# Performance work log

Hardware: AMD Instinct MI355X
Metric: run time of the kernel (lower is better)

Reference implementation:

```python
import jax, jax.numpy as jnp
import numpy as np

BLOCK = 128  # block_size=(128,128) from MoeFP8Matmul
E, H, I = 8, 2048, 2816  # experts, hidden, intermediate
T, K = 512, 2  # tokens, top-k

_FP8 = getattr(jnp, "float8_e4m3fn", jnp.float32)

def _dequant(w, s):
    # w: [N, Kd] fp8 values (stored fp32), s: [N//128, Kd//128] inverse scales
    s_full = jnp.repeat(jnp.repeat(s, BLOCK, axis=-2), BLOCK, axis=-1)
    return w * s_full

def setup_inputs() -> dict:
    key = jax.random.key(0)
    ks = jax.random.split(key, 7)
    x = jax.random.normal(ks[0], (T, H), dtype=jnp.float32)
    topk_ids = jax.random.randint(ks[1], (T, K), 0, E, dtype=jnp.int64)
    topk_weights = jax.random.uniform(ks[2], (T, K), dtype=jnp.float32)
    # fp8-representable weight values (round-trip through e4m3)
    w13 = (jax.random.normal(ks[3], (E, 2 * I, H), dtype=jnp.float32) * 0.5)
    w13_fp8 = w13.astype(_FP8).astype(jnp.float32)
    w2 = (jax.random.normal(ks[4], (E, H, I), dtype=jnp.float32) * 0.5)
    w2_fp8 = w2.astype(_FP8).astype(jnp.float32)
    w13_scale = jax.random.uniform(ks[5], (E, (2 * I) // BLOCK, H // BLOCK),
                                   dtype=jnp.float32, minval=0.5, maxval=1.5)
    w2_scale = jax.random.uniform(ks[6], (E, H // BLOCK, I // BLOCK),
                                  dtype=jnp.float32, minval=0.5, maxval=1.5)
    return {"x": x, "topk_ids": topk_ids, "topk_weights": topk_weights,
            "w13_fp8": w13_fp8, "w13_scale": w13_scale,
            "w2_fp8": w2_fp8, "w2_scale": w2_scale}

def reference(x, topk_ids, topk_weights, w13_fp8, w13_scale, w2_fp8, w2_scale):
    # Per-expert block-FP8 dequant then grouped SwiGLU MoE GEMM, weighted-summed by router.
    out = jnp.zeros_like(x)
    for e in range(E):  # small fixed expert count
        W13 = _dequant(w13_fp8[e], w13_scale[e])   # [2I, H]
        W2 = _dequant(w2_fp8[e], w2_scale[e])      # [H, I]
        h = x @ W13.T                              # [T, 2I]
        gate, up = jnp.split(h, 2, axis=-1)
        act = jax.nn.silu(gate) * up               # [T, I]
        oe = act @ W2.T                            # [T, H]
        coef = jnp.sum(jnp.where(topk_ids == e, topk_weights, 0.0), axis=-1)  # [T]
        out = out + coef[:, None] * oe
    return out
```

## Files before the change

### kernel.cpp

```cpp
#include <hip/hip_runtime.h>
#include <hip/hip_bf16.h>
#include <cstdint>
#include <cstddef>

#define E_   8
#define H_   2048
#define I_   2816
#define T_   512
#define NPAIR 1024

#define TM   192
#define TN   32
#define BK   64
#define LDSB 72
#define MT_  3

typedef __attribute__((ext_vector_type(8))) short          bf16x8;
typedef __attribute__((ext_vector_type(4))) float          f32x4;
typedef __attribute__((ext_vector_type(8))) unsigned short u16x8;

__device__ __forceinline__ unsigned short f2bf(float f){
  union { float f; unsigned u; } a; a.f = f;
  unsigned u = a.u;
  unsigned r = u + 0x7fffu + ((u >> 16) & 1u);
  return (unsigned short)(r >> 16);
}

__global__ void route_kernel(const int* __restrict__ ids,
                             int* __restrict__ offs, int* __restrict__ ptok,
                             int* __restrict__ sop){
  __shared__ int scnt[E_];
  __shared__ int scur[E_];
  const int tid = threadIdx.x;
  if (tid < E_) scnt[tid] = 0;
  __syncthreads();
  const int e = ids[tid];
  atomicAdd(&scnt[e], 1);
  __syncthreads();
  if (tid == 0){
    int s = 0;
    for (int i = 0; i < E_; i++){ offs[i] = s; scur[i] = s; s += scnt[i]; }
    offs[E_] = s;
  }
  __syncthreads();
  const int pos = atomicAdd(&scur[e], 1);
  ptok[pos] = tid >> 1;
  sop[tid]  = pos;
}

__global__ void prep_kernel(const float* __restrict__ x, const int* __restrict__ ptok,
                            unsigned short* __restrict__ xg){
  const int slot = blockIdx.x;
  const int tok  = ptok[slot];
  const int k0   = threadIdx.x * 8;
  const float4 v0 = *(const float4*)(x + (size_t)tok*H_ + k0);
  const float4 v1 = *(const float4*)(x + (size_t)tok*H_ + k0 + 4);
  u16x8 o;
  o[0]=f2bf(v0.x); o[1]=f2bf(v0.y); o[2]=f2bf(v0.z); o[3]=f2bf(v0.w);
  o[4]=f2bf(v1.x); o[5]=f2bf(v1.y); o[6]=f2bf(v1.z); o[7]=f2bf(v1.w);
  *(u16x8*)(xg + (size_t)slot*H_ + k0) = o;
}

__global__ __launch_bounds__(256, 3)
void gemm1_kernel(const unsigned short* __restrict__ xg, const float* __restrict__ w13,
                  const float* __restrict__ s13, const int* __restrict__ offs,
                  unsigned short* __restrict__ act)
{
  const int e   = blockIdx.z;
  const int off = offs[e];
  const int cnt = offs[e+1] - off;
  const int m0  = blockIdx.y * TM;
  if (m0 >= cnt) return;
  const int rows = min(TM, cnt - m0);
  const int nb   = blockIdx.x * TN;

  __shared__ __align__(16) unsigned short Bs[2][2*TN][LDSB];

  const int tid  = threadIdx.x;
  const int wave = tid >> 6;
  const int lane = tid & 63;
  const int quad = lane >> 4;
  const int l16  = lane & 15;

  const float* w13e = w13 + (size_t)e * (2*I_) * H_;
  const float* s13e = s13 + (size_t)e * (2*I_/128) * (H_/128);

  const int br = tid >> 2;
  const int bc = tid & 3;
  const int grow = (br < TN) ? (nb + br) : (I_ + nb + (br - TN));
  const float* bp = w13e + (size_t)grow * H_;
  const int srow  = ((br < TN) ? 0 : (I_/128)) + (nb >> 7);

  const unsigned short* aP[MT_];
  #pragma unroll
  for (int mt = 0; mt < MT_; mt++){
    int sl = off + m0 + wave*(TM/4) + mt*16 + l16;
    sl = min(sl, NPAIR - 1);
    aP[mt] = xg + (size_t)sl * H_;
  }

  f32x4 acc[2][MT_][2];
  #pragma unroll
  for (int h = 0; h < 2; h++)
    #pragma unroll
    for (int mt = 0; mt < MT_; mt++)
      #pragma unroll
      for (int nt = 0; nt < 2; nt++)
        acc[h][mt][nt] = (f32x4){0.f, 0.f, 0.f, 0.f};

  float4 pb[4];
  #pragma unroll
  for (int j = 0; j < 4; j++) pb[j] = *(const float4*)(bp + (bc*4 + j)*4);
  {
    const float s = s13e[srow*(H_/128)];
    u16x8 wv0, wv1;
    wv0[0]=f2bf(pb[0].x*s); wv0[1]=f2bf(pb[0].y*s); wv0[2]=f2bf(pb[0].z*s); wv0[3]=f2bf(pb[0].w*s);
    wv0[4]=f2bf(pb[1].x*s); wv0[5]=f2bf(pb[1].y*s); wv0[6]=f2bf(pb[1].z*s); wv0[7]=f2bf(pb[1].w*s);
    wv1[0]=f2bf(pb[2].x*s); wv1[1]=f2bf(pb[2].y*s); wv1[2]=f2bf(pb[2].z*s); wv1[3]=f2bf(pb[2].w*s);
    wv1[4]=f2bf(pb[3].x*s); wv1[5]=f2bf(pb[3].y*s); wv1[6]=f2bf(pb[3].z*s); wv1[7]=f2bf(pb[3].w*s);
    *(u16x8*)&Bs[0][br][bc*16]     = wv0;
    *(u16x8*)&Bs[0][br][bc*16 + 8] = wv1;
  }
  __syncthreads();

  int cur = 0;
  for (int kb = 0; kb < H_; kb += BK){
    const bool more = (kb + BK) < H_;
    if (more){
      #pragma unroll
      for (int j = 0; j < 4; j++) pb[j] = *(const float4*)(bp + kb + BK + (bc*4 + j)*4);
    }
    bf16x8 af[2][MT_];
    #pragma unroll
    for (int kk = 0; kk < 2; kk++)
      #pragma unroll
      for (int mt = 0; mt < MT_; mt++)
        af[kk][mt] = *(const bf16x8*)(aP[mt] + kb + kk*32 + quad*8);

    #pragma unroll
    for (int kk = 0; kk < 2; kk++){
      #pragma unroll
      for (int hh = 0; hh < 2; hh++){
        #pragma unroll
        for (int nt = 0; nt < 2; nt++){
          bf16x8 bv = *(const bf16x8*)&Bs[cur][hh*TN + nt*16 + l16][kk*32 + quad*8];
          #pragma unroll
          for (int mt = 0; mt < MT_; mt++)
            acc[hh][mt][nt] = __builtin_amdgcn_mfma_f32_16x16x32_bf16(af[kk][mt], bv, acc[hh][mt][nt], 0, 0, 0);
        }
      }
    }
    if (more){
      const float s = s13e[srow*(H_/128) + ((kb + BK) >> 7)];
      u16x8 wv0, wv1;
      wv0[0]=f2bf(pb[0].x*s); wv0[1]=f2bf(pb[0].y*s); wv0[2]=f2bf(pb[0].z*s); wv0[3]=f2bf(pb[0].w*s);
      wv0[4]=f2bf(pb[1].x*s); wv0[5]=f2bf(pb[1].y*s); wv0[6]=f2bf(pb[1].z*s); wv0[7]=f2bf(pb[1].w*s);
      wv1[0]=f2bf(pb[2].x*s); wv1[1]=f2bf(pb[2].y*s); wv1[2]=f2bf(pb[2].z*s); wv1[3]=f2bf(pb[2].w*s);
      wv1[4]=f2bf(pb[3].x*s); wv1[5]=f2bf(pb[3].y*s); wv1[6]=f2bf(pb[3].z*s); wv1[7]=f2bf(pb[3].w*s);
      *(u16x8*)&Bs[cur^1][br][bc*16]     = wv0;
      *(u16x8*)&Bs[cur^1][br][bc*16 + 8] = wv1;
      __syncthreads();
      cur ^= 1;
    }
  }

  #pragma unroll
  for (int mt = 0; mt < MT_; mt++){
    #pragma unroll
    for (int nt = 0; nt < 2; nt++){
      #pragma unroll
      for (int r = 0; r < 4; r++){
        const int m = wave*(TM/4) + mt*16 + quad*4 + r;
        if (m < rows){
          const float g = acc[0][mt][nt][r];
          const float u = acc[1][mt][nt][r];
          const float sg = g / (1.f + __expf(-g));
          act[(size_t)(off + m0 + m)*I_ + (nb + nt*16 + l16)] = f2bf(sg * u);
        }
      }
    }
  }
}

__global__ __launch_bounds__(256, 4)
void gemm2_kernel(const unsigned short* __restrict__ act, const float* __restrict__ w2,
                  const float* __restrict__ s2, const int* __restrict__ offs,
                  float* __restrict__ buf)
{
  const int e   = blockIdx.z;
  const int off = offs[e];
  const int cnt = offs[e+1] - off;
  const int m0  = blockIdx.y * TM;
  if (m0 >= cnt) return;
  const int rows = min(TM, cnt - m0);
  const int nb   = blockIdx.x * TN;

  __shared__ __align__(16) unsigned short Bs[2][TN][LDSB];

  const int tid  = threadIdx.x;
  const int wave = tid >> 6;
  const int lane = tid & 63;
  const int quad = lane >> 4;
  const int l16  = lane & 15;

  const float* w2e = w2 + (size_t)e * H_ * I_;
  const float* s2e = s2 + (size_t)e * (H_/128) * (I_/128);

  const int br = tid >> 3;
  const int bc = tid & 7;
  const float* bp = w2e + (size_t)(nb + br) * I_;
  const int srow  = nb >> 7;

  const unsigned short* aP[MT_];
  #pragma unroll
  for (int mt = 0; mt < MT_; mt++){
    int sl = off + m0 + wave*(TM/4) + mt*16 + l16;
    sl = min(sl, NPAIR - 1);
    aP[mt] = act + (size_t)sl * I_;
  }

  f32x4 acc[MT_][2];
  #pragma unroll
  for (int mt = 0; mt < MT_; mt++)
    #pragma unroll
    for (int nt = 0; nt < 2; nt++)
      acc[mt][nt] = (f32x4){0.f, 0.f, 0.f, 0.f};

  float4 pb[2];
  #pragma unroll
  for (int j = 0; j < 2; j++) pb[j] = *(const float4*)(bp + (bc*2 + j)*4);
  {
    const float s = s2e[srow*(I_/128)];
    u16x8 wv;
    wv[0]=f2bf(pb[0].x*s); wv[1]=f2bf(pb[0].y*s); wv[2]=f2bf(pb[0].z*s); wv[3]=f2bf(pb[0].w*s);
    wv[4]=f2bf(pb[1].x*s); wv[5]=f2bf(pb[1].y*s); wv[6]=f2bf(pb[1].z*s); wv[7]=f2bf(pb[1].w*s);
    *(u16x8*)&Bs[0][br][bc*8] = wv;
  }
  __syncthreads();

  int cur = 0;
  for (int kb = 0; kb < I_; kb += BK){
    const bool more = (kb + BK) < I_;
    if (more){
      #pragma unroll
      for (int j = 0; j < 2; j++) pb[j] = *(const float4*)(bp + kb + BK + (bc*2 + j)*4);
    }
    bf16x8 af[2][MT_];
    #pragma unroll
    for (int kk = 0; kk < 2; kk++)
      #pragma unroll
      for (int mt = 0; mt < MT_; mt++)
        af[kk][mt] = *(const bf16x8*)(aP[mt] + kb + kk*32 + quad*8);

    #pragma unroll
    for (int kk = 0; kk < 2; kk++){
      #pragma unroll
      for (int nt = 0; nt < 2; nt++){
        bf16x8 bv = *(const bf16x8*)&Bs[cur][nt*16 + l16][kk*32 + quad*8];
        #pragma unroll
        for (int mt = 0; mt < MT_; mt++)
          acc[mt][nt] = __builtin_amdgcn_mfma_f32_16x16x32_bf16(af[kk][mt], bv, acc[mt][nt], 0, 0, 0);
      }
    }
    if (more){
      const float s = s2e[srow*(I_/128) + ((kb + BK) >> 7)];
      u16x8 wv;
      wv[0]=f2bf(pb[0].x*s); wv[1]=f2bf(pb[0].y*s); wv[2]=f2bf(pb[0].z*s); wv[3]=f2bf(pb[0].w*s);
      wv[4]=f2bf(pb[1].x*s); wv[5]=f2bf(pb[1].y*s); wv[6]=f2bf(pb[1].z*s); wv[7]=f2bf(pb[1].w*s);
      *(u16x8*)&Bs[cur^1][br][bc*8] = wv;
      __syncthreads();
      cur ^= 1;
    }
  }

  #pragma unroll
  for (int mt = 0; mt < MT_; mt++){
    #pragma unroll
    for (int nt = 0; nt < 2; nt++){
      #pragma unroll
      for (int r = 0; r < 4; r++){
        const int m = wave*(TM/4) + mt*16 + quad*4 + r;
        if (m < rows)
          buf[(size_t)(off + m0 + m)*H_ + (nb + nt*16 + l16)] = acc[mt][nt][r];
      }
    }
  }
}

__global__ void combine_kernel(const float* __restrict__ buf, const int* __restrict__ sop,
                               const float* __restrict__ tw, float* __restrict__ out){
  const int gid = blockIdx.x*256 + threadIdx.x;
  const int t = gid >> 9;
  const int c = gid & 511;
  const int s0 = sop[2*t], s1 = sop[2*t+1];
  const float w0 = tw[2*t], w1 = tw[2*t+1];
  const float4 v0 = ((const float4*)buf)[(size_t)s0*(H_/4) + c];
  const float4 v1 = ((const float4*)buf)[(size_t)s1*(H_/4) + c];
  float4 o;
  o.x = w0*v0.x + w1*v1.x;
  o.y = w0*v0.y + w1*v1.y;
  o.z = w0*v0.z + w1*v1.z;
  o.w = w0*v0.w + w1*v1.w;
  ((float4*)out)[gid] = o;
}

extern "C" void kernel_launch(void* const* d_in, const int* in_sizes, int n_in,
                              void* d_out, int out_size, void* d_ws, size_t ws_size,
                              hipStream_t stream){
  const float* x   = (const float*)d_in[0];
  const int*   ids = (const int*)  d_in[1];
  const float* tw  = (const float*)d_in[2];
  const float* w13 = (const float*)d_in[3];
  const float* s13 = (const float*)d_in[4];
  const float* w2  = (const float*)d_in[5];
  const float* s2  = (const float*)d_in[6];
  float* out = (float*)d_out;

  char* ws = (char*)d_ws;
  int* offs = (int*)ws;
  int* ptok = (int*)(ws + 64);
  int* sop  = (int*)(ws + 64 + 4096);
  unsigned short* xg  = (unsigned short*)(ws + 16384);
  float*          buf = (float*)(ws + 16384);
  unsigned short* act = (unsigned short*)(ws + 16384 + (size_t)NPAIR*H_*4);

  route_kernel  <<<1, NPAIR, 0, stream>>>(ids, offs, ptok, sop);
  prep_kernel   <<<NPAIR, 256, 0, stream>>>(x, ptok, xg);
  gemm1_kernel  <<<dim3(I_/TN, (NPAIR + TM - 1)/TM, E_), 256, 0, stream>>>(xg, w13, s13, offs, act);
  gemm2_kernel  <<<dim3(H_/TN, (NPAIR + TM - 1)/TM, E_), 256, 0, stream>>>(act, w2, s2, offs, buf);
  combine_kernel<<<(T_*H_/4)/256, 256, 0, stream>>>(buf, sop, tw, out);
}
```

Measured before the change: 793.0 us.

## Software-pipeline both MoE GEMMs with register double-buffering and LDS-only barriers

Restructures the K loops of both grouped GEMMs into a 2-way unrolled pipeline. Weight tiles are prefetched two steps ahead and activation fragments one step ahead in registers, and __syncthreads is replaced by a barrier that waits only on LDS counters, so global loads can stay in flight across the barrier. The bf16 conversion now uses packed HIP intrinsics, pointer offsets are hoisted out of the loop, and gemm2's launch bound drops to 3 blocks per SM to make room for the extra registers. The risk is higher register pressure and lower occupancy.

```diff
diff --git a/kernel.cpp b/kernel.cpp
--- a/kernel.cpp
+++ b/kernel.cpp
@@ -24,6 +24,20 @@
   unsigned u = a.u;
   unsigned r = u + 0x7fffu + ((u >> 16) & 1u);
   return (unsigned short)(r >> 16);
+}
+
+__device__ __forceinline__ void cvt4(u16x8& dst, int base, const float4 v, float s){
+  __hip_bfloat162 p0 = __float22bfloat162_rn(float2{v.x*s, v.y*s});
+  __hip_bfloat162 p1 = __float22bfloat162_rn(float2{v.z*s, v.w*s});
+  union { __hip_bfloat162 b; unsigned u; } a0{p0}, a1{p1};
+  dst[base+0] = (unsigned short)(a0.u & 0xffff);
+  dst[base+1] = (unsigned short)(a0.u >> 16);
+  dst[base+2] = (unsigned short)(a1.u & 0xffff);
+  dst[base+3] = (unsigned short)(a1.u >> 16);
+}
+
+__device__ __forceinline__ void sync_lds(){
+  asm volatile("s_waitcnt lgkmcnt(0)\n\ts_barrier" ::: "memory");
 }
 
 __global__ void route_kernel(const int* __restrict__ ids,
@@ -56,8 +70,8 @@
   const float4 v0 = *(const float4*)(x + (size_t)tok*H_ + k0);
   const float4 v1 = *(const float4*)(x + (size_t)tok*H_ + k0 + 4);
   u16x8 o;
-  o[0]=f2bf(v0.x); o[1]=f2bf(v0.y); o[2]=f2bf(v0.z); o[3]=f2bf(v0.w);
-  o[4]=f2bf(v1.x); o[5]=f2bf(v1.y); o[6]=f2bf(v1.z); o[7]=f2bf(v1.w);
+  cvt4(o, 0, v0, 1.f);
+  cvt4(o, 4, v1, 1.f);
   *(u16x8*)(xg + (size_t)slot*H_ + k0) = o;
 }
 
@@ -88,15 +102,15 @@
   const int br = tid >> 2;
   const int bc = tid & 3;
   const int grow = (br < TN) ? (nb + br) : (I_ + nb + (br - TN));
-  const float* bp = w13e + (size_t)grow * H_;
-  const int srow  = ((br < TN) ? 0 : (I_/128)) + (nb >> 7);
+  const float* bp = w13e + (size_t)grow * H_ + bc*16;
+  const int srow  = (((br < TN) ? 0 : (I_/128)) + (nb >> 7)) * (H_/128);
 
   const unsigned short* aP[MT_];
   #pragma unroll
   for (int mt = 0; mt < MT_; mt++){
     int sl = off + m0 + wave*(TM/4) + mt*16 + l16;
     sl = min(sl, NPAIR - 1);
-    aP[mt] = xg + (size_t)sl * H_;
+    aP[mt] = xg + (size_t)sl * H_ + quad*8;
   }
 
   f32x4 acc[2][MT_][2];
@@ -108,60 +122,60 @@
       for (int nt = 0; nt < 2; nt++)
         acc[h][mt][nt] = (f32x4){0.f, 0.f, 0.f, 0.f};
 
-  float4 pb[4];
-  #pragma unroll
-  for (int j = 0; j < 4; j++) pb[j] = *(const float4*)(bp + (bc*4 + j)*4);
-  {
-    const float s = s13e[srow*(H_/128)];
-    u16x8 wv0, wv1;
-    wv0[0]=f2bf(pb[0].x*s); wv0[1]=f2bf(pb[0].y*s); wv0[2]=f2bf(pb[0].z*s); wv0[3]=f2bf(pb[0].w*s);
-    wv0[4]=f2bf(pb[1].x*s); wv0[5]=f2bf(pb[1].y*s); wv0[6]=f2bf(pb[1].z*s); wv0[7]=f2bf(pb[1].w*s);
-    wv1[0]=f2bf(pb[2].x*s); wv1[1]=f2bf(pb[2].y*s); wv1[2]=f2bf(pb[2].z*s); wv1[3]=f2bf(pb[2].w*s);
-    wv1[4]=f2bf(pb[3].x*s); wv1[5]=f2bf(pb[3].y*s); wv1[6]=f2bf(pb[3].z*s); wv1[7]=f2bf(pb[3].w*s);
-    *(u16x8*)&Bs[0][br][bc*16]     = wv0;
-    *(u16x8*)&Bs[0][br][bc*16 + 8] = wv1;
-  }
-  __syncthreads();
-
-  int cur = 0;
-  for (int kb = 0; kb < H_; kb += BK){
-    const bool more = (kb + BK) < H_;
-    if (more){
-      #pragma unroll
-      for (int j = 0; j < 4; j++) pb[j] = *(const float4*)(bp + kb + BK + (bc*4 + j)*4);
-    }
-    bf16x8 af[2][MT_];
+  float4 R0[4], R1[4];
+  bf16x8 A0[2][MT_], A1[2][MT_];
+  float  sE, sO;
+
+  auto loadB = [&](int t, float4* R){
+    const float* p = bp + t*BK;
+    #pragma unroll
+    for (int j = 0; j < 4; j++) R[j] = *(const float4*)(p + j*4);
+  };
+  auto loadA = [&](int t, bf16x8 (*A)[MT_]){
     #pragma unroll
     for (int kk = 0; kk < 2; kk++)
       #pragma unroll
       for (int mt = 0; mt < MT_; mt++)
-        af[kk][mt] = *(const bf16x8*)(aP[mt] + kb + kk*32 + quad*8);
-
-    #pragma unroll
-    for (int kk = 0; kk < 2; kk++){
-      #pragma unroll
-      for (int hh = 0; hh < 2; hh++){
+        A[kk][mt] = *(const bf16x8*)(aP[mt] + t*BK + kk*32);
+  };
+  auto storeB = [&](const float4* R, float s, int buf){
+    u16x8 w0, w1;
+    cvt4(w0, 0, R[0], s); cvt4(w0, 4, R[1], s);
+    cvt4(w1, 0, R[2], s); cvt4(w1, 4, R[3], s);
+    *(u16x8*)&Bs[buf][br][bc*16]     = w0;
+    *(u16x8*)&Bs[buf][br][bc*16 + 8] = w1;
+  };
+  auto mfma = [&](int buf, bf16x8 (*A)[MT_]){
+    #pragma unroll
+    for (int kk = 0; kk < 2; kk++)
+      #pragma unroll
+      for (int hh = 0; hh < 2; hh++)
         #pragma unroll
         for (int nt = 0; nt < 2; nt++){
-          bf16x8 bv = *(const bf16x8*)&Bs[cur][hh*TN + nt*16 + l16][kk*32 + quad*8];
+          bf16x8 bv = *(const bf16x8*)&Bs[buf][hh*TN + nt*16 + l16][kk*32 + quad*8];
           #pragma unroll
           for (int mt = 0; mt < MT_; mt++)
-            acc[hh][mt][nt] = __builtin_amdgcn_mfma_f32_16x16x32_bf16(af[kk][mt], bv, acc[hh][mt][nt], 0, 0, 0);
+            acc[hh][mt][nt] = __builtin_amdgcn_mfma_f32_16x16x32_bf16(A[kk][mt], bv, acc[hh][mt][nt], 0, 0, 0);
         }
-      }
-    }
-    if (more){
-      const float s = s13e[srow*(H_/128) + ((kb + BK) >> 7)];
-      u16x8 wv0, wv1;
-      wv0[0]=f2bf(pb[0].x*s); wv0[1]=f2bf(pb[0].y*s); wv0[2]=f2bf(pb[0].z*s); wv0[3]=f2bf(pb[0].w*s);
-      wv0[4]=f2bf(pb[1].x*s); wv0[5]=f2bf(pb[1].y*s); wv0[6]=f2bf(pb[1].z*s); wv0[7]=f2bf(pb[1].w*s);
-      wv1[0]=f2bf(pb[2].x*s); wv1[1]=f2bf(pb[2].y*s); wv1[2]=f2bf(pb[2].z*s); wv1[3]=f2bf(pb[2].w*s);
-      wv1[4]=f2bf(pb[3].x*s); wv1[5]=f2bf(pb[3].y*s); wv1[6]=f2bf(pb[3].z*s); wv1[7]=f2bf(pb[3].w*s);
-      *(u16x8*)&Bs[cur^1][br][bc*16]     = wv0;
-      *(u16x8*)&Bs[cur^1][br][bc*16 + 8] = wv1;
-      __syncthreads();
-      cur ^= 1;
-    }
+  };
+
+  const int NITER = H_/BK;
+  loadB(0, R0); sE = s13e[srow];
+  loadB(1, R1); sO = s13e[srow];
+  loadA(0, A0);
+  storeB(R0, sE, 0);
+  sync_lds();
+
+  for (int i = 0; i < NITER; i += 2){
+    if (i+2 < NITER){ loadB(i+2, R0); sE = s13e[srow + ((i+2) >> 1)]; }
+    loadA(i+1, A1);
+    mfma(0, A0);
+    storeB(R1, sO, 1);
+    sync_lds();
+    if (i+3 < NITER){ loadB(i+3, R1); sO = s13e[srow + ((i+3) >> 1)]; }
+    if (i+2 < NITER) loadA(i+2, A0);
+    mfma(1, A1);
+    if (i+2 < NITER){ storeB(R0, sE, 0); sync_lds(); }
   }
 
   #pragma unroll
@@ -182,7 +196,7 @@
   }
 }
 
-__global__ __launch_bounds__(256, 4)
+__global__ __launch_bounds__(256, 3)
 void gemm2_kernel(const unsigned short* __restrict__ act, const float* __restrict__ w2,
                   const float* __restrict__ s2, const int* __restrict__ offs,
                   float* __restrict__ buf)
@@ -208,15 +222,15 @@
 
   const int br = tid >> 3;
   const int bc = tid & 7;
-  const float* bp = w2e + (size_t)(nb + br) * I_;
-  const int srow  = nb >> 7;
+  const float* bp = w2e + (size_t)(nb + br) * I_ + bc*8;
+  const int srow  = (nb >> 7) * (I_/128);
 
   const unsigned short* aP[MT_];
   #pragma unroll
   for (int mt = 0; mt < MT_; mt++){
     int sl = off + m0 + wave*(TM/4) + mt*16 + l16;
     sl = min(sl, NPAIR - 1);
-    aP[mt] = act + (size_t)sl * I_;
+    aP[mt] = act + (size_t)sl * I_ + quad*8;
   }
 
   f32x4 acc[MT_][2];
@@ -226,51 +240,56 @@
     for (int nt = 0; nt < 2; nt++)
       acc[mt][nt] = (f32x4){0.f, 0.f, 0.f, 0.f};
 
-  float4 pb[2];
-  #pragma unroll
-  for (int j = 0; j < 2; j++) pb[j] = *(const float4*)(bp + (bc*2 + j)*4);
-  {
-    const float s = s2e[srow*(I_/128)];
-    u16x8 wv;
-    wv[0]=f2bf(pb[0].x*s); wv[1]=f2bf(pb[0].y*s); wv[2]=f2bf(pb[0].z*s); wv[3]=f2bf(pb[0].w*s);
-    wv[4]=f2bf(pb[1].x*s); wv[5]=f2bf(pb[1].y*s); wv[6]=f2bf(pb[1].z*s); wv[7]=f2bf(pb[1].w*s);
-    *(u16x8*)&Bs[0][br][bc*8] = wv;
-  }
-  __syncthreads();
-
-  int cur = 0;
-  for (int kb = 0; kb < I_; kb += BK){
-    const bool more = (kb + BK) < I_;
-    if (more){
-      #pragma unroll
-      for (int j = 0; j < 2; j++) pb[j] = *(const float4*)(bp + kb + BK + (bc*2 + j)*4);
-    }
-    bf16x8 af[2][MT_];
+  float4 R0[2], R1[2];
+  bf16x8 A0[2][MT_], A1[2][MT_];
+  float  sE, sO;
+
+  auto loadB = [&](int t, float4* R){
+    const float* p = bp + t*BK;
+    #pragma unroll
+    for (int j = 0; j < 2; j++) R[j] = *(const float4*)(p + j*4);
+  };
+  auto loadA = [&](int t, bf16x8 (*A)[MT_]){
     #pragma unroll
     for (int kk = 0; kk < 2; kk++)
       #pragma unroll
       for (int mt = 0; mt < MT_; mt++)
-        af[kk][mt] = *(const bf16x8*)(aP[mt] + kb + kk*32 + quad*8);
-
-    #pragma unroll
-    for (int kk = 0; kk < 2; kk++){
+        A[kk][mt] = *(const bf16x8*)(aP[mt] + t*BK + kk*32);
+  };
+  auto storeB = [&](const float4* R, float s, int buf_i){
+    u16x8 w0;
+    cvt4(w0, 0, R[0], s); cvt4(w0, 4, R[1], s);
+    *(u16x8*)&Bs[buf_i][br][bc*8] = w0;
+  };
+  auto mfma = [&](int buf_i, bf16x8 (*A)[MT_]){
+    #pragma unroll
+    for (int kk = 0; kk < 2; kk++)
       #pragma unroll
       for (int nt = 0; nt < 2; nt++){
-        bf16x8 bv = *(const bf16x8*)&Bs[cur][nt*16 + l16][kk*32 + quad*8];
+        bf16x8 bv = *(const bf16x8*)&Bs[buf_i][nt*16 + l16][kk*32 + quad*8];
         #pragma unroll
         for (int mt = 0; mt < MT_; mt++)
-          acc[mt][nt] = __builtin_amdgcn_mfma_f32_16x16x32_bf16(af[kk][mt], bv, acc[mt][nt], 0, 0, 0);
+          acc[mt][nt] = __builtin_amdgcn_mfma_f32_16x16x32_bf16(A[kk][mt], bv, acc[mt][nt], 0, 0, 0);
       }
-    }
-    if (more){
-      const float s = s2e[srow*(I_/128) + ((kb + BK) >> 7)];
-      u16x8 wv;
-      wv[0]=f2bf(pb[0].x*s); wv[1]=f2bf(pb[0].y*s); wv[2]=f2bf(pb[0].z*s); wv[3]=f2bf(pb[0].w*s);
-      wv[4]=f2bf(pb[1].x*s); wv[5]=f2bf(pb[1].y*s); wv[6]=f2bf(pb[1].z*s); wv[7]=f2bf(pb[1].w*s);
-      *(u16x8*)&Bs[cur^1][br][bc*8] = wv;
-      __syncthreads();
-      cur ^= 1;
-    }
+  };
+
+  const int NITER = I_/BK;
+  loadB(0, R0); sE = s2e[srow];
+  loadB(1, R1); sO = s2e[srow];
+  loadA(0, A0);
+  storeB(R0, sE, 0);
+  sync_lds();
+
+  for (int i = 0; i < NITER; i += 2){
+    if (i+2 < NITER){ loadB(i+2, R0); sE = s2e[srow + ((i+2) >> 1)]; }
+    loadA(i+1, A1);
+    mfma(0, A0);
+    storeB(R1, sO, 1);
+    sync_lds();
+    if (i+3 < NITER){ loadB(i+3, R1); sO = s2e[srow + ((i+3) >> 1)]; }
+    if (i+2 < NITER) loadA(i+2, A0);
+    mfma(1, A1);
+    if (i+2 < NITER){ storeB(R0, sE, 0); sync_lds(); }
   }
 
   #pragma unroll
```

After: 726.1 us. 1.09x faster.
